# Kernel tuning notes

Hardware: AMD Instinct MI355X
Metric: run time of the kernel (lower is better)

The kernel has to match this reference:

```python
import jax, jax.numpy as jnp
import numpy as np

B, L, H = 32, 2048, 512


def setup_inputs() -> dict:
    key = jax.random.key(0)
    k1, k2, k3, k4, k5, k6 = jax.random.split(key, 6)
    scale = 1.0 / np.sqrt(H)
    return {
        "query": jax.random.normal(k1, (B, H), dtype=jnp.float32),
        "ref": jax.random.normal(k2, (B, L, H), dtype=jnp.float32),
        "mask": jax.random.randint(k3, (B, L), 0, 2) == 1,
        # learned params (torch Linear weight layout: [out, in]; apply as x @ W.T)
        "W_ref": jax.random.normal(k4, (H, H), dtype=jnp.float32) * scale,
        "W_q": jax.random.normal(k5, (H, H), dtype=jnp.float32) * scale,
        "v": jax.random.normal(k6, (H,), dtype=jnp.float32) * scale,
    }


def reference(query, ref, mask, W_ref, W_q, v):
    scale = 1.0 / np.sqrt(H)
    # additive (Bahdanau) scores: v^T tanh(W_ref ref + W_q q)
    encoded_ref = jnp.einsum("blh,oh->blo", ref, W_ref)          # (B, L, H)
    encoded_q = jnp.einsum("bh,oh->bo", query, W_q)[:, None, :]  # (B, 1, H)
    scores = jnp.einsum("blh,h->bl", jnp.tanh(encoded_ref + encoded_q), v)
    scores = scores * scale
    scores = jnp.where(mask, -1e9, scores)
    attn = jax.nn.softmax(scores, axis=1)                         # (B, L)
    glimpse = jnp.einsum("bl,blh->bh", attn, ref)                 # (B, H)
    return glimpse, scores
```

## Files before the change

kernel.cpp:

```cpp
#include <hip/hip_runtime.h>
#include <hip/hip_bf16.h>
#include <cstdint>

typedef __attribute__((ext_vector_type(4))) float f32x4;
typedef __attribute__((ext_vector_type(8))) short s16x8;

#define NB   32
#define NL   2048
#define NH   512
#define NM   (NB * NL)
#define SCALE 0.04419417382415922f

__device__ __forceinline__ ushort f2bf(float f) {
    __hip_bfloat16 b = __float2bfloat16(f);
    return *reinterpret_cast<ushort*>(&b);
}
__device__ __forceinline__ unsigned long long pack4(float4 f) {
    union { ushort u[4]; unsigned long long v; } p;
    p.u[0] = f2bf(f.x); p.u[1] = f2bf(f.y); p.u[2] = f2bf(f.z); p.u[3] = f2bf(f.w);
    return p.v;
}

#define GL16(g, l)                                                         \
    __builtin_amdgcn_global_load_lds(                                      \
        (const __attribute__((address_space(1))) unsigned int*)(g),        \
        (__attribute__((address_space(3))) unsigned int*)(l), 16, 0, 0)

__global__ __launch_bounds__(256) void k_pre(const float* __restrict__ W,
                                             ushort* __restrict__ Wb,
                                             const float* __restrict__ query,
                                             const float* __restrict__ Wq,
                                             float* __restrict__ eq) {
    int bid = blockIdx.x;
    int t = threadIdx.x;
    if (bid < 64) {
        const float4* F = (const float4*)W;
        unsigned long long* U = (unsigned long long*)Wb;
        int base = bid * 1024 + t;
        float4 f[4];
#pragma unroll
        for (int k = 0; k < 4; ++k) f[k] = F[base + k * 256];
#pragma unroll
        for (int k = 0; k < 4; ++k) U[base + k * 256] = pack4(f[k]);
    } else {
        __shared__ float q[NH];
        int b = bid - 64;
        q[t] = query[b * NH + t];
        q[t + 256] = query[b * NH + t + 256];
        __syncthreads();
#pragma unroll
        for (int half = 0; half < 2; ++half) {
            int o = t + half * 256;
            const float4* w = (const float4*)(Wq + (size_t)o * NH);
            float acc = 0.f;
#pragma unroll 4
            for (int i = 0; i < NH / 4; ++i) {
                float4 x = w[i];
                acc += q[4 * i] * x.x + q[4 * i + 1] * x.y + q[4 * i + 2] * x.z + q[4 * i + 3] * x.w;
            }
            eq[b * NH + o] = acc;
        }
    }
}

__global__ __launch_bounds__(512, 4) void k_gemm_full(const float* __restrict__ ref,
                                                      const ushort* __restrict__ Wb,
                                                      const float* __restrict__ eq,
                                                      const float* __restrict__ v,
                                                      const int* __restrict__ mask,
                                                      float* __restrict__ out_sc) {
    __shared__ char smem[81920];
    ushort* Bs0 = (ushort*)smem;
    ushort* Bs1 = (ushort*)(smem + 32768);
    float*  As0 = (float*)(smem + 65536);
    float*  As1 = (float*)(smem + 73728);

    int tid = threadIdx.x;
    int lane = tid & 63, wid = tid >> 6;
    int blk = blockIdx.x;
    int m0g = blk << 6;
    int b = blk >> 5;

    f32x4 acc[4][4];
#pragma unroll
    for (int i = 0; i < 4; ++i)
#pragma unroll
        for (int j = 0; j < 4; ++j) acc[i][j] = (f32x4)(0.f);

    const ushort* bglob = Wb + ((size_t)(wid * 64) + (lane >> 2)) * NH
                             + (((lane & 3) ^ ((lane >> 3) & 3)) << 3);
    const float* aglob = ref + (size_t)(m0g + wid * 8 + (lane >> 3)) * NH
                             + (((lane & 7) ^ ((lane >> 3) & 7)) << 2);

    int lr = lane & 15, kq = lane >> 4;
    int bbase = (wid * 64 + lr) * 32 + ((kq ^ ((lr >> 1) & 3)) << 3);
    int arow = lr * 32;
    int ac0 = (((2 * kq) ^ (lr & 7)) << 2);
    int ac1 = (((2 * kq + 1) ^ (lr & 7)) << 2);

#define STAGE(Bsb, Asb, kt)                                           \
    {   GL16(bglob + (kt) * 32,            Bsb + (wid * 64) * 32);    \
        GL16(bglob + (kt) * 32 + 16 * NH,  Bsb + (wid * 64 + 16) * 32); \
        GL16(bglob + (kt) * 32 + 32 * NH,  Bsb + (wid * 64 + 32) * 32); \
        GL16(bglob + (kt) * 32 + 48 * NH,  Bsb + (wid * 64 + 48) * 32); \
        GL16(aglob + (kt) * 32,            Asb + (wid * 8) * 32); }

#define READ_COMPUTE(Bsb, Asb)                                                   \
    {   s16x8 bfr[4], af[4];                                                     \
        _Pragma("unroll")                                                        \
        for (int f = 0; f < 4; ++f) bfr[f] = *(const s16x8*)&Bsb[bbase + f * 512]; \
        _Pragma("unroll")                                                        \
        for (int f = 0; f < 4; ++f) {                                            \
            float4 a0 = *(const float4*)(Asb + arow + f * 512 + ac0);            \
            float4 a1 = *(const float4*)(Asb + arow + f * 512 + ac1);            \
            union { ushort u[8]; s16x8 v; } p;                                   \
            p.u[0] = f2bf(a0.x); p.u[1] = f2bf(a0.y);                            \
            p.u[2] = f2bf(a0.z); p.u[3] = f2bf(a0.w);                            \
            p.u[4] = f2bf(a1.x); p.u[5] = f2bf(a1.y);                            \
            p.u[6] = f2bf(a1.z); p.u[7] = f2bf(a1.w);                            \
            af[f] = p.v;                                                         \
        }                                                                        \
        _Pragma("unroll")                                                        \
        for (int fr = 0; fr < 4; ++fr)                                           \
            _Pragma("unroll")                                                    \
            for (int fc = 0; fc < 4; ++fc)                                       \
                acc[fr][fc] = __builtin_amdgcn_mfma_f32_16x16x32_bf16(           \
                    af[fr], bfr[fc], acc[fr][fc], 0, 0, 0);                      \
    }

    STAGE(Bs0, As0, 0)
    __syncthreads();

    for (int t2 = 0; t2 < 8; ++t2) {
        int k0 = 2 * t2;
        STAGE(Bs1, As1, k0 + 1)
        READ_COMPUTE(Bs0, As0)
        __syncthreads();
        if (k0 + 2 < 16) STAGE(Bs0, As0, k0 + 2)
        READ_COMPUTE(Bs1, As1)
        __syncthreads();
    }
#undef STAGE
#undef READ_COMPUTE

    float* sc_red = (float*)smem;
    const float* eqb = eq + b * NH;
    float vv[4], ee[4];
#pragma unroll
    for (int fc = 0; fc < 4; ++fc) {
        int c = wid * 64 + fc * 16 + lr;
        vv[fc] = v[c];
        ee[fc] = eqb[c];
    }
#pragma unroll
    for (int fr = 0; fr < 4; ++fr) {
#pragma unroll
        for (int reg = 0; reg < 4; ++reg) {
            float s = 0.f;
#pragma unroll
            for (int fc = 0; fc < 4; ++fc) {
                float x = acc[fr][fc][reg] + ee[fc];
                float t = 1.f - 2.f / (__expf(2.f * x) + 1.f);
                s += vv[fc] * t;
            }
            s += __shfl_xor(s, 1);
            s += __shfl_xor(s, 2);
            s += __shfl_xor(s, 4);
            s += __shfl_xor(s, 8);
            if (lr == 0) sc_red[wid * 64 + fr * 16 + kq * 4 + reg] = s;
        }
    }
    __syncthreads();
    if (tid < 64) {
        float t = 0.f;
#pragma unroll
        for (int w = 0; w < 8; ++w) t += sc_red[w * 64 + tid];
        t *= SCALE;
        int rg = m0g + tid;
        if (mask[rg] != 0) t = -1e9f;
        out_sc[rg] = t;
    }
}

__global__ __launch_bounds__(256) void k_smglp(const float* __restrict__ scores,
                                               const float* __restrict__ ref,
                                               float* __restrict__ glp) {
    int sp = blockIdx.x, b = blockIdx.y;
    int tid = threadIdx.x;
    int lane = tid & 63, wid = tid >> 6;
    __shared__ float red[4];
    __shared__ float asl[128];
    float sc[8];
    float mx = -3.4e38f;
#pragma unroll
    for (int i = 0; i < 8; ++i) {
        sc[i] = scores[b * NL + i * 256 + tid];
        mx = fmaxf(mx, sc[i]);
    }
#pragma unroll
    for (int o = 32; o >= 1; o >>= 1) mx = fmaxf(mx, __shfl_xor(mx, o));
    if (lane == 0) red[wid] = mx;
    __syncthreads();
    mx = fmaxf(fmaxf(red[0], red[1]), fmaxf(red[2], red[3]));
    __syncthreads();
    float ls = 0.f;
#pragma unroll
    for (int i = 0; i < 8; ++i) {
        float e = __expf(sc[i] - mx);
        ls += e;
        if (i == (sp >> 1) && (tid >> 7) == (sp & 1)) asl[tid & 127] = e;
    }
#pragma unroll
    for (int o = 32; o >= 1; o >>= 1) ls += __shfl_xor(ls, o);
    if (lane == 0) red[wid] = ls;
    __syncthreads();
    float inv = 1.f / (red[0] + red[1] + red[2] + red[3]);

    const float* rb = ref + ((size_t)b * NL + sp * 128) * NH;
    float2 acc = make_float2(0.f, 0.f);
#pragma unroll 4
    for (int l = 0; l < 128; ++l) {
        float a = asl[l];
        float2 r = ((const float2*)(rb + (size_t)l * NH))[tid];
        acc.x += a * r.x;
        acc.y += a * r.y;
    }
    acc.x *= inv;
    acc.y *= inv;
    ((float2*)(glp + (size_t)(sp * NB + b) * NH))[tid] = acc;
}

__global__ __launch_bounds__(256) void k_gred(const float* __restrict__ glp,
                                              float* __restrict__ out_gl) {
    int idx = blockIdx.x * 256 + threadIdx.x;
    float s = 0.f;
#pragma unroll
    for (int sp = 0; sp < 16; ++sp) s += glp[sp * (NB * NH) + idx];
    out_gl[idx] = s;
}

extern "C" void kernel_launch(void* const* d_in, const int* in_sizes, int n_in,
                              void* d_out, int out_size, void* d_ws, size_t ws_size,
                              hipStream_t stream) {
    const float* query = (const float*)d_in[0];
    const float* ref   = (const float*)d_in[1];
    const int*   mask  = (const int*)d_in[2];
    const float* W_ref = (const float*)d_in[3];
    const float* W_q   = (const float*)d_in[4];
    const float* v     = (const float*)d_in[5];

    float* out_gl = (float*)d_out;
    float* out_sc = out_gl + NB * NH;

    char* w = (char*)d_ws;
    ushort* wW = (ushort*)w;
    float* eq  = (float*)(w + 524288);
    float* glp = (float*)(w + 589824);

    k_pre<<<96, 256, 0, stream>>>(W_ref, wW, query, W_q, eq);
    k_gemm_full<<<1024, 512, 0, stream>>>(ref, wW, eq, v, mask, out_sc);
    k_smglp<<<dim3(16, NB), 256, 0, stream>>>(out_sc, ref, glp);
    k_gred<<<64, 256, 0, stream>>>(glp, out_gl);
}
```

Measured before the change: 124.9 us.

## Restructure GEMM main loop with explicit vmcnt waits, split barriers and MFMA priority

The K-loop is rewritten so both LDS buffers are prefetched up front. Each step waits with explicit vmcnt counts, reads and converts fragments into registers, then issues the next global-to-LDS stage before running the MFMAs at raised wave priority. The goal is to overlap global loads with matrix compute and drop the full __syncthreads after each compute phase. The XOR swizzle on the B (weight) tile in LDS is also removed, which may add LDS bank conflicts on the B fragment reads. The hand-tuned waitcnt values depend on exact load counts and are fragile.

```diff
diff --git a/kernel.cpp b/kernel.cpp
--- a/kernel.cpp
+++ b/kernel.cpp
@@ -87,13 +87,12 @@
 #pragma unroll
         for (int j = 0; j < 4; ++j) acc[i][j] = (f32x4)(0.f);
 
-    const ushort* bglob = Wb + ((size_t)(wid * 64) + (lane >> 2)) * NH
-                             + (((lane & 3) ^ ((lane >> 3) & 3)) << 3);
+    const ushort* bglob = Wb + ((size_t)(wid * 64) + (lane >> 2)) * NH + ((lane & 3) << 3);
     const float* aglob = ref + (size_t)(m0g + wid * 8 + (lane >> 3)) * NH
                              + (((lane & 7) ^ ((lane >> 3) & 7)) << 2);
 
     int lr = lane & 15, kq = lane >> 4;
-    int bbase = (wid * 64 + lr) * 32 + ((kq ^ ((lr >> 1) & 3)) << 3);
+    int bbase = (wid * 64 + lr) * 32 + (kq << 3);
     int arow = lr * 32;
     int ac0 = (((2 * kq) ^ (lr & 7)) << 2);
     int ac1 = (((2 * kq + 1) ^ (lr & 7)) << 2);
@@ -105,43 +104,78 @@
         GL16(bglob + (kt) * 32 + 48 * NH,  Bsb + (wid * 64 + 48) * 32); \
         GL16(aglob + (kt) * 32,            Asb + (wid * 8) * 32); }
 
-#define READ_COMPUTE(Bsb, Asb)                                                   \
-    {   s16x8 bfr[4], af[4];                                                     \
+#define READ_CVT(Bsb, Asb)                                                       \
+    _Pragma("unroll")                                                            \
+    for (int f = 0; f < 4; ++f) bfr[f] = *(const s16x8*)&Bsb[bbase + f * 512];   \
+    _Pragma("unroll")                                                            \
+    for (int f = 0; f < 4; ++f) {                                                \
+        float4 a0 = *(const float4*)(Asb + arow + f * 512 + ac0);                \
+        float4 a1 = *(const float4*)(Asb + arow + f * 512 + ac1);                \
+        union { ushort u[8]; s16x8 v; } p;                                       \
+        p.u[0] = f2bf(a0.x); p.u[1] = f2bf(a0.y);                                \
+        p.u[2] = f2bf(a0.z); p.u[3] = f2bf(a0.w);                                \
+        p.u[4] = f2bf(a1.x); p.u[5] = f2bf(a1.y);                                \
+        p.u[6] = f2bf(a1.z); p.u[7] = f2bf(a1.w);                                \
+        af[f] = p.v;                                                             \
+    }
+
+#define MFMA_ALL()                                                               \
+    __builtin_amdgcn_s_setprio(1);                                               \
+    _Pragma("unroll")                                                            \
+    for (int fr = 0; fr < 4; ++fr)                                               \
         _Pragma("unroll")                                                        \
-        for (int f = 0; f < 4; ++f) bfr[f] = *(const s16x8*)&Bsb[bbase + f * 512]; \
-        _Pragma("unroll")                                                        \
-        for (int f = 0; f < 4; ++f) {                                            \
-            float4 a0 = *(const float4*)(Asb + arow + f * 512 + ac0);            \
-            float4 a1 = *(const float4*)(Asb + arow + f * 512 + ac1);            \
-            union { ushort u[8]; s16x8 v; } p;                                   \
-            p.u[0] = f2bf(a0.x); p.u[1] = f2bf(a0.y);                            \
-            p.u[2] = f2bf(a0.z); p.u[3] = f2bf(a0.w);                            \
-            p.u[4] = f2bf(a1.x); p.u[5] = f2bf(a1.y);                            \
-            p.u[6] = f2bf(a1.z); p.u[7] = f2bf(a1.w);                            \
-            af[f] = p.v;                                                         \
-        }                                                                        \
-        _Pragma("unroll")                                                        \
-        for (int fr = 0; fr < 4; ++fr)                                           \
-            _Pragma("unroll")                                                    \
-            for (int fc = 0; fc < 4; ++fc)                                       \
-                acc[fr][fc] = __builtin_amdgcn_mfma_f32_16x16x32_bf16(           \
-                    af[fr], bfr[fc], acc[fr][fc], 0, 0, 0);                      \
-    }
+        for (int fc = 0; fc < 4; ++fc)                                           \
+            acc[fr][fc] = __builtin_amdgcn_mfma_f32_16x16x32_bf16(               \
+                af[fr], bfr[fc], acc[fr][fc], 0, 0, 0);                          \
+    __builtin_amdgcn_s_setprio(0);
 
     STAGE(Bs0, As0, 0)
-    __syncthreads();
-
-    for (int t2 = 0; t2 < 8; ++t2) {
-        int k0 = 2 * t2;
-        STAGE(Bs1, As1, k0 + 1)
-        READ_COMPUTE(Bs0, As0)
-        __syncthreads();
-        if (k0 + 2 < 16) STAGE(Bs0, As0, k0 + 2)
-        READ_COMPUTE(Bs1, As1)
-        __syncthreads();
+    STAGE(Bs1, As1, 1)
+
+#pragma unroll 1
+    for (int t2 = 0; t2 < 7; ++t2) {
+        {
+            s16x8 bfr[4], af[4];
+            asm volatile("s_waitcnt vmcnt(5)" ::: "memory");
+            __builtin_amdgcn_s_barrier();
+            READ_CVT(Bs0, As0)
+            asm volatile("s_waitcnt lgkmcnt(0)" ::: "memory");
+            __builtin_amdgcn_sched_barrier(0);
+            __builtin_amdgcn_s_barrier();
+            STAGE(Bs0, As0, 2 * t2 + 2)
+            MFMA_ALL()
+        }
+        {
+            s16x8 bfr[4], af[4];
+            asm volatile("s_waitcnt vmcnt(5)" ::: "memory");
+            __builtin_amdgcn_s_barrier();
+            READ_CVT(Bs1, As1)
+            asm volatile("s_waitcnt lgkmcnt(0)" ::: "memory");
+            __builtin_amdgcn_sched_barrier(0);
+            __builtin_amdgcn_s_barrier();
+            STAGE(Bs1, As1, 2 * t2 + 3)
+            MFMA_ALL()
+        }
+    }
+    {
+        s16x8 bfr[4], af[4];
+        asm volatile("s_waitcnt vmcnt(5)" ::: "memory");
+        __builtin_amdgcn_s_barrier();
+        READ_CVT(Bs0, As0)
+        MFMA_ALL()
+    }
+    {
+        s16x8 bfr[4], af[4];
+        asm volatile("s_waitcnt vmcnt(0)" ::: "memory");
+        __builtin_amdgcn_s_barrier();
+        READ_CVT(Bs1, As1)
+        MFMA_ALL()
     }
 #undef STAGE
-#undef READ_COMPUTE
+#undef READ_CVT
+#undef MFMA_ALL
+
+    __syncthreads();
 
     float* sc_red = (float*)smem;
     const float* eqb = eq + b * NH;
```

After: 120.7 us. -3.4%, faster.

## Pre-convert ref to bf16 and use 256x256 GEMM tiles with split-N partial scores

Applied to the files above, without the earlier changes.

Adds a conversion pass that writes ref as bf16 into workspace, so the GEMM stages bf16 A tiles directly instead of converting fp32 in the inner loop. The GEMM moves from 64-row tiles covering all 512 outputs to 256x256 tiles with an 8x4 fragment layout, an XCD-aware block mapping, explicit waitcnt/barrier pipelining and setprio. The two N-halves write partial scores, which the softmax kernel sums, scales and masks; the glimpse pass also reads the bf16 ref. This trades an extra full read and half-size write of ref for cheaper GEMM loads, at the cost of bf16 rounding in the glimpse.

```diff
diff --git a/kernel.cpp b/kernel.cpp
--- a/kernel.cpp
+++ b/kernel.cpp
@@ -15,6 +15,9 @@
     __hip_bfloat16 b = __float2bfloat16(f);
     return *reinterpret_cast<ushort*>(&b);
 }
+__device__ __forceinline__ float bf2f(unsigned u) {
+    union { unsigned u; float f; } a; a.u = u << 16; return a.f;
+}
 __device__ __forceinline__ unsigned long long pack4(float4 f) {
     union { ushort u[4]; unsigned long long v; } p;
     p.u[0] = f2bf(f.x); p.u[1] = f2bf(f.y); p.u[2] = f2bf(f.z); p.u[3] = f2bf(f.w);
@@ -26,25 +29,24 @@
         (const __attribute__((address_space(1))) unsigned int*)(g),        \
         (__attribute__((address_space(3))) unsigned int*)(l), 16, 0, 0)
 
-__global__ __launch_bounds__(256) void k_pre(const float* __restrict__ W,
-                                             ushort* __restrict__ Wb,
-                                             const float* __restrict__ query,
-                                             const float* __restrict__ Wq,
-                                             float* __restrict__ eq) {
+__global__ __launch_bounds__(256) void k_conv(const float* __restrict__ ref,
+                                              ushort* __restrict__ refb,
+                                              const float* __restrict__ W,
+                                              ushort* __restrict__ Wb,
+                                              const float* __restrict__ query,
+                                              const float* __restrict__ Wq,
+                                              float* __restrict__ eq) {
     int bid = blockIdx.x;
     int t = threadIdx.x;
-    if (bid < 64) {
-        const float4* F = (const float4*)W;
-        unsigned long long* U = (unsigned long long*)Wb;
-        int base = bid * 1024 + t;
-        float4 f[4];
-#pragma unroll
-        for (int k = 0; k < 4; ++k) f[k] = F[base + k * 256];
-#pragma unroll
-        for (int k = 0; k < 4; ++k) U[base + k * 256] = pack4(f[k]);
+    if (bid < 32768) {
+        int g = bid * 256 + t;
+        ((unsigned long long*)refb)[g] = pack4(((const float4*)ref)[g]);
+    } else if (bid < 33024) {
+        int g = (bid - 32768) * 256 + t;
+        ((unsigned long long*)Wb)[g] = pack4(((const float4*)W)[g]);
     } else {
         __shared__ float q[NH];
-        int b = bid - 64;
+        int b = bid - 33024;
         q[t] = query[b * NH + t];
         q[t + 256] = query[b * NH + t + 256];
         __syncthreads();
@@ -63,97 +65,112 @@
     }
 }
 
-__global__ __launch_bounds__(512, 4) void k_gemm_full(const float* __restrict__ ref,
-                                                      const ushort* __restrict__ Wb,
-                                                      const float* __restrict__ eq,
-                                                      const float* __restrict__ v,
-                                                      const int* __restrict__ mask,
-                                                      float* __restrict__ out_sc) {
-    __shared__ char smem[81920];
-    ushort* Bs0 = (ushort*)smem;
-    ushort* Bs1 = (ushort*)(smem + 32768);
-    float*  As0 = (float*)(smem + 65536);
-    float*  As1 = (float*)(smem + 73728);
+__global__ __launch_bounds__(512, 1) void k_gemm8(const ushort* __restrict__ refb,
+                                                  const ushort* __restrict__ Wb,
+                                                  const float* __restrict__ eq,
+                                                  const float* __restrict__ v,
+                                                  float* __restrict__ part) {
+    __shared__ ushort smem[65536];
+    ushort* As0 = smem;
+    ushort* Bs0 = smem + 16384;
+    ushort* As1 = smem + 32768;
+    ushort* Bs1 = smem + 49152;
 
     int tid = threadIdx.x;
     int lane = tid & 63, wid = tid >> 6;
-    int blk = blockIdx.x;
-    int m0g = blk << 6;
-    int b = blk >> 5;
-
-    f32x4 acc[4][4];
-#pragma unroll
-    for (int i = 0; i < 4; ++i)
+    int wr = wid >> 2, wc = wid & 3;
+
+    int phys = blockIdx.x;
+    int xcd = phys & 7, slot = phys >> 3;
+    int mt = xcd * 32 + (slot >> 1);
+    int nt = slot & 1;
+    int m0g = mt << 8, n0 = nt << 8;
+    int b = mt >> 3;
+
+    f32x4 acc[8][4];
+#pragma unroll
+    for (int i = 0; i < 8; ++i)
 #pragma unroll
         for (int j = 0; j < 4; ++j) acc[i][j] = (f32x4)(0.f);
 
-    const ushort* bglob = Wb + ((size_t)(wid * 64) + (lane >> 2)) * NH
-                             + (((lane & 3) ^ ((lane >> 3) & 3)) << 3);
-    const float* aglob = ref + (size_t)(m0g + wid * 8 + (lane >> 3)) * NH
-                             + (((lane & 7) ^ ((lane >> 3) & 7)) << 2);
-
     int lr = lane & 15, kq = lane >> 4;
-    int bbase = (wid * 64 + lr) * 32 + ((kq ^ ((lr >> 1) & 3)) << 3);
-    int arow = lr * 32;
-    int ac0 = (((2 * kq) ^ (lr & 7)) << 2);
-    int ac1 = (((2 * kq + 1) ^ (lr & 7)) << 2);
-
-#define STAGE(Bsb, Asb, kt)                                           \
-    {   GL16(bglob + (kt) * 32,            Bsb + (wid * 64) * 32);    \
-        GL16(bglob + (kt) * 32 + 16 * NH,  Bsb + (wid * 64 + 16) * 32); \
-        GL16(bglob + (kt) * 32 + 32 * NH,  Bsb + (wid * 64 + 32) * 32); \
-        GL16(bglob + (kt) * 32 + 48 * NH,  Bsb + (wid * 64 + 48) * 32); \
-        GL16(aglob + (kt) * 32,            Asb + (wid * 8) * 32); }
-
-#define READ_COMPUTE(Bsb, Asb)                                                   \
-    {   s16x8 bfr[4], af[4];                                                     \
-        _Pragma("unroll")                                                        \
-        for (int f = 0; f < 4; ++f) bfr[f] = *(const s16x8*)&Bsb[bbase + f * 512]; \
-        _Pragma("unroll")                                                        \
-        for (int f = 0; f < 4; ++f) {                                            \
-            float4 a0 = *(const float4*)(Asb + arow + f * 512 + ac0);            \
-            float4 a1 = *(const float4*)(Asb + arow + f * 512 + ac1);            \
-            union { ushort u[8]; s16x8 v; } p;                                   \
-            p.u[0] = f2bf(a0.x); p.u[1] = f2bf(a0.y);                            \
-            p.u[2] = f2bf(a0.z); p.u[3] = f2bf(a0.w);                            \
-            p.u[4] = f2bf(a1.x); p.u[5] = f2bf(a1.y);                            \
-            p.u[6] = f2bf(a1.z); p.u[7] = f2bf(a1.w);                            \
-            af[f] = p.v;                                                         \
-        }                                                                        \
-        _Pragma("unroll")                                                        \
-        for (int fr = 0; fr < 4; ++fr)                                           \
-            _Pragma("unroll")                                                    \
-            for (int fc = 0; fc < 4; ++fc)                                       \
-                acc[fr][fc] = __builtin_amdgcn_mfma_f32_16x16x32_bf16(           \
-                    af[fr], bfr[fc], acc[fr][fc], 0, 0, 0);                      \
-    }
-
-    STAGE(Bs0, As0, 0)
-    __syncthreads();
-
-    for (int t2 = 0; t2 < 8; ++t2) {
-        int k0 = 2 * t2;
-        STAGE(Bs1, As1, k0 + 1)
-        READ_COMPUTE(Bs0, As0)
-        __syncthreads();
-        if (k0 + 2 < 16) STAGE(Bs0, As0, k0 + 2)
-        READ_COMPUTE(Bs1, As1)
-        __syncthreads();
-    }
+    int l7 = lr & 7;
+    int sA0 = ((kq) ^ l7) << 3;
+    int sA1 = ((4 + kq) ^ l7) << 3;
+    int abase0 = (wr * 128 + lr) * 64;
+    int bbase0 = (wc * 64 + lr) * 64;
+
+#define STAGE(Asb, Bsb, kt)                                                    \
+    {   _Pragma("unroll")                                                      \
+        for (int ho = 0; ho < 4; ++ho) {                                       \
+            int br = (ho >> 1) * 128 + wid * 16 + (ho & 1) * 8;                \
+            int rl = br + (lane >> 3);                                         \
+            int gc = (lane & 7) ^ (rl & 7);                                    \
+            GL16(refb + (size_t)(m0g + rl) * NH + (kt) * 64 + gc * 8, (Asb) + br * 64); \
+            GL16(Wb   + (size_t)(n0  + rl) * NH + (kt) * 64 + gc * 8, (Bsb) + br * 64); \
+        } }
+
+#define TILE_BODY(Asb, Bsb)                                                    \
+    {   s16x8 bq[4][2];                                                        \
+        _Pragma("unroll")                                                      \
+        for (int fc = 0; fc < 4; ++fc) {                                       \
+            bq[fc][0] = *(const s16x8*)&(Bsb)[bbase0 + fc * 1024 + sA0];       \
+            bq[fc][1] = *(const s16x8*)&(Bsb)[bbase0 + fc * 1024 + sA1];       \
+        }                                                                      \
+        __builtin_amdgcn_s_setprio(1);                                         \
+        _Pragma("unroll")                                                      \
+        for (int fr = 0; fr < 8; ++fr) {                                       \
+            s16x8 a0 = *(const s16x8*)&(Asb)[abase0 + fr * 1024 + sA0];        \
+            s16x8 a1 = *(const s16x8*)&(Asb)[abase0 + fr * 1024 + sA1];        \
+            _Pragma("unroll")                                                  \
+            for (int fc = 0; fc < 4; ++fc) {                                   \
+                acc[fr][fc] = __builtin_amdgcn_mfma_f32_16x16x32_bf16(         \
+                    a0, bq[fc][0], acc[fr][fc], 0, 0, 0);                      \
+                acc[fr][fc] = __builtin_amdgcn_mfma_f32_16x16x32_bf16(         \
+                    a1, bq[fc][1], acc[fr][fc], 0, 0, 0);                      \
+            }                                                                  \
+        }                                                                      \
+        __builtin_amdgcn_s_setprio(0);                                         \
+    }
+
+#define TILE(Asb, Bsb, WAITN, DOSTAGE, Asn, Bsn, kstage)                       \
+    {   asm volatile("s_waitcnt vmcnt(" #WAITN ")" ::: "memory");              \
+        __builtin_amdgcn_s_barrier();                                          \
+        TILE_BODY(Asb, Bsb)                                                    \
+        asm volatile("s_waitcnt lgkmcnt(0)" ::: "memory");                     \
+        __builtin_amdgcn_s_barrier();                                          \
+        if (DOSTAGE) STAGE(Asn, Bsn, kstage)                                   \
+    }
+
+    STAGE(As0, Bs0, 0)
+    STAGE(As1, Bs1, 1)
+
+    TILE(As0, Bs0, 8, 1, As0, Bs0, 2)
+    TILE(As1, Bs1, 8, 1, As1, Bs1, 3)
+    TILE(As0, Bs0, 8, 1, As0, Bs0, 4)
+    TILE(As1, Bs1, 8, 1, As1, Bs1, 5)
+    TILE(As0, Bs0, 8, 1, As0, Bs0, 6)
+    TILE(As1, Bs1, 8, 1, As1, Bs1, 7)
+    TILE(As0, Bs0, 8, 0, As0, Bs0, 0)
+    TILE(As1, Bs1, 0, 0, As1, Bs1, 0)
+
 #undef STAGE
-#undef READ_COMPUTE
+#undef TILE_BODY
+#undef TILE
+
+    __syncthreads();
 
     float* sc_red = (float*)smem;
     const float* eqb = eq + b * NH;
     float vv[4], ee[4];
 #pragma unroll
     for (int fc = 0; fc < 4; ++fc) {
-        int c = wid * 64 + fc * 16 + lr;
+        int c = n0 + wc * 64 + fc * 16 + lr;
         vv[fc] = v[c];
         ee[fc] = eqb[c];
     }
 #pragma unroll
-    for (int fr = 0; fr < 4; ++fr) {
+    for (int fr = 0; fr < 8; ++fr) {
 #pragma unroll
         for (int reg = 0; reg < 4; ++reg) {
             float s = 0.f;
@@ -167,23 +184,24 @@
             s += __shfl_xor(s, 2);
             s += __shfl_xor(s, 4);
             s += __shfl_xor(s, 8);
-            if (lr == 0) sc_red[wid * 64 + fr * 16 + kq * 4 + reg] = s;
+            if (lr == 0) sc_red[wid * 128 + fr * 16 + kq * 4 + reg] = s;
         }
     }
     __syncthreads();
-    if (tid < 64) {
-        float t = 0.f;
-#pragma unroll
-        for (int w = 0; w < 8; ++w) t += sc_red[w * 64 + tid];
-        t *= SCALE;
-        int rg = m0g + tid;
-        if (mask[rg] != 0) t = -1e9f;
-        out_sc[rg] = t;
-    }
-}
-
-__global__ __launch_bounds__(256) void k_smglp(const float* __restrict__ scores,
-                                               const float* __restrict__ ref,
+    if (tid < 256) {
+        int row = tid;
+        int g0 = (row >> 7) * 4;
+        int rl = row & 127;
+        float s = sc_red[(g0 + 0) * 128 + rl] + sc_red[(g0 + 1) * 128 + rl]
+                + sc_red[(g0 + 2) * 128 + rl] + sc_red[(g0 + 3) * 128 + rl];
+        part[(size_t)nt * NM + m0g + row] = s;
+    }
+}
+
+__global__ __launch_bounds__(256) void k_smglp(const float* __restrict__ part,
+                                               const int* __restrict__ mask,
+                                               const ushort* __restrict__ refb,
+                                               float* __restrict__ out_sc,
                                                float* __restrict__ glp) {
     int sp = blockIdx.x, b = blockIdx.y;
     int tid = threadIdx.x;
@@ -194,8 +212,12 @@
     float mx = -3.4e38f;
 #pragma unroll
     for (int i = 0; i < 8; ++i) {
-        sc[i] = scores[b * NL + i * 256 + tid];
-        mx = fmaxf(mx, sc[i]);
+        int m = b * NL + i * 256 + tid;
+        float s = (part[m] + part[NM + m]) * SCALE;
+        if (mask[m] != 0) s = -1e9f;
+        if (sp == 0) out_sc[m] = s;
+        sc[i] = s;
+        mx = fmaxf(mx, s);
     }
 #pragma unroll
     for (int o = 32; o >= 1; o >>= 1) mx = fmaxf(mx, __shfl_xor(mx, o));
@@ -216,14 +238,14 @@
     __syncthreads();
     float inv = 1.f / (red[0] + red[1] + red[2] + red[3]);
 
-    const float* rb = ref + ((size_t)b * NL + sp * 128) * NH;
+    const ushort* rb = refb + ((size_t)b * NL + sp * 128) * NH;
     float2 acc = make_float2(0.f, 0.f);
 #pragma unroll 4
     for (int l = 0; l < 128; ++l) {
         float a = asl[l];
-        float2 r = ((const float2*)(rb + (size_t)l * NH))[tid];
-        acc.x += a * r.x;
-        acc.y += a * r.y;
+        unsigned r = ((const unsigned*)(rb + (size_t)l * NH))[tid];
+        acc.x += a * bf2f(r & 0xFFFFu);
+        acc.y += a * bf2f(r >> 16);
     }
     acc.x *= inv;
     acc.y *= inv;
@@ -253,12 +275,14 @@
     float* out_sc = out_gl + NB * NH;
 
     char* w = (char*)d_ws;
-    ushort* wW = (ushort*)w;
-    float* eq  = (float*)(w + 524288);
-    float* glp = (float*)(w + 589824);
-
-    k_pre<<<96, 256, 0, stream>>>(W_ref, wW, query, W_q, eq);
-    k_gemm_full<<<1024, 512, 0, stream>>>(ref, wW, eq, v, mask, out_sc);
-    k_smglp<<<dim3(16, NB), 256, 0, stream>>>(out_sc, ref, glp);
+    ushort* wW   = (ushort*)w;
+    float*  eq   = (float*)(w + 524288);
+    ushort* refb = (ushort*)(w + 589824);
+    float*  part = (float*)(w + 589824 + 67108864);
+    float*  glp  = (float*)(w + 589824 + 67108864 + 524288);
+
+    k_conv<<<33056, 256, 0, stream>>>(ref, refb, W_ref, wW, query, W_q, eq);
+    k_gemm8<<<512, 512, 0, stream>>>(refb, wW, eq, v, part);
+    k_smglp<<<dim3(16, NB), 256, 0, stream>>>(part, mask, refb, out_sc, glp);
     k_gred<<<64, 256, 0, stream>>>(glp, out_gl);
 }
```

Result: slower. 130.4 us (+4.4%).
